# Performance work log

Measured on AMD Instinct MI355X. Metric: run time of the kernel, lower is better.

The kernel has to match this reference:

```python
import jax, jax.numpy as jnp
import numpy as np
from jax import lax

B, N, K = 8, 4096, 16          # clouds, points per cloud, knn neighbors
RATIO = 0.5
M = int(N * RATIO)             # sampled points per cloud (fps ratio)
C_IN, C_OUT = 64, 128
EPS = 1e-5                      # BatchNorm eps


def setup_inputs() -> dict:
    key = jax.random.key(0)
    ks = jax.random.split(key, 4)
    x = jax.random.normal(ks[0], (B * N, C_IN), jnp.float32)
    pos = jax.random.uniform(ks[1], (B * N, 3), jnp.float32)
    batch = jnp.repeat(jnp.arange(B, dtype=jnp.int32), N)
    W = jax.random.normal(ks[2], (C_IN, C_OUT), jnp.float32) / np.sqrt(C_IN).astype(np.float32)
    b = jnp.zeros((C_OUT,), jnp.float32)
    gamma = jnp.ones((C_OUT,), jnp.float32)
    beta = jnp.zeros((C_OUT,), jnp.float32)
    return {"x": x, "pos": pos, "batch": batch, "W": W, "b": b, "gamma": gamma, "beta": beta}


def _fps(pos_c):
    # Farthest point sampling on one cloud. pos_c: [N,3] -> [M] local indices.
    # Deterministic start at index 0 (reference for torch_cluster.fps).
    def step(carry, _):
        dmin, last = carry
        d = jnp.sum((pos_c - pos_c[last]) ** 2, axis=-1)   # [N]
        dmin = jnp.minimum(dmin, d)
        nxt = jnp.argmax(dmin).astype(jnp.int32)
        return (dmin, nxt), last
    init = (jnp.full((pos_c.shape[0],), jnp.inf, pos_c.dtype), jnp.int32(0))
    _, idx = lax.scan(step, init, None, length=M)
    return idx


def _knn(pos_c, qpos_c):
    # k nearest original points for each sampled point. [N,3],[M,3] -> [M,K].
    d = jnp.sum((qpos_c[:, None, :] - pos_c[None, :, :]) ** 2, axis=-1)  # [M,N]
    _, idx = lax.top_k(-d, K)
    return idx


def reference(x, pos, batch, W, b, gamma, beta):
    pos_b = pos.reshape(B, N, 3)
    fps_idx = jax.vmap(_fps)(pos_b)                                       # [B,M]
    new_pos_b = jnp.take_along_axis(pos_b, fps_idx[:, :, None], axis=1)   # [B,M,3]
    nbr = jax.vmap(_knn)(pos_b, new_pos_b)                                # [B,M,K]

    # mlp: Linear -> BatchNorm1d (training-mode batch stats) -> GELU
    h = x @ W + b                                                         # [B*N,C_OUT]
    mu = jnp.mean(h, axis=0)
    var = jnp.mean((h - mu) ** 2, axis=0)
    h = (h - mu) * lax.rsqrt(var + EPS) * gamma + beta
    h = jax.nn.gelu(h, approximate=False)
    h_b = h.reshape(B, N, C_OUT)

    # gather neighbor features; scatter-max over edge_index[0] == max over K
    # (each sampled point has exactly K incoming edges)
    feats = jax.vmap(lambda hb, nb: hb[nb])(h_b, nbr)                     # [B,M,K,C_OUT]
    new_x = jnp.max(feats, axis=2).reshape(B * M, C_OUT)
    new_pos = new_pos_b.reshape(B * M, 3)
    new_batch = jnp.repeat(jnp.arange(B, dtype=batch.dtype), M)
    return (new_x, new_pos, new_batch)
```

## Files before the change

### kernel.cpp

```cpp
#include <hip/hip_runtime.h>
#include <math.h>

#define NB 8
#define NN 4096
#define MM 2048
#define KNN_K 16
#define CIN 64
#define COUT 128
#define BN_EPS 1e-5f
#define NWORK 128
#define NTILES 512

typedef float v2f __attribute__((ext_vector_type(2)));

__device__ __forceinline__ v2f pk_add(v2f a, v2f b) {
  v2f r;
  asm("v_pk_add_f32 %0, %1, %2" : "=v"(r) : "v"(a), "v"(b));
  return r;
}
__device__ __forceinline__ v2f pk_mul(v2f a, v2f b) {
  v2f r;
  asm("v_pk_mul_f32 %0, %1, %2" : "=v"(r) : "v"(a), "v"(b));
  return r;
}

__device__ __forceinline__ double pack_key(float d, unsigned code) {
  return __longlong_as_double(
      (long long)(((unsigned long long)__float_as_uint(d) << 32) | code));
}
__device__ __forceinline__ unsigned unpack_code(double v) {
  return (unsigned)((unsigned long long)__double_as_longlong(v) &
                    0xFFFFFFFFull);
}

__device__ __forceinline__ float sqdist_np(float dx, float dy, float dz) {
  return __fadd_rn(__fadd_rn(__fmul_rn(dx, dx), __fmul_rn(dy, dy)),
                   __fmul_rn(dz, dz));
}

__device__ __forceinline__ void bar_lds_only() {
  asm volatile("s_waitcnt lgkmcnt(0)\n\ts_barrier" ::: "memory");
}

#define DPP_MAX_LEVEL(best, ctrl, rmask)                                     \
  {                                                                          \
    const int _lo = __builtin_amdgcn_update_dpp(                             \
        __double2loint(best), __double2loint(best), (ctrl), (rmask), 0xf,    \
        false);                                                              \
    const int _hi = __builtin_amdgcn_update_dpp(                             \
        __double2hiint(best), __double2hiint(best), (ctrl), (rmask), 0xf,    \
        false);                                                              \
    best = fmax(best, __hiloint2double(_hi, _lo));                           \
  }
#define DPP_MIN_LEVEL(best, ctrl, rmask)                                     \
  {                                                                          \
    const int _lo = __builtin_amdgcn_update_dpp(                             \
        __double2loint(best), __double2loint(best), (ctrl), (rmask), 0xf,    \
        false);                                                              \
    const int _hi = __builtin_amdgcn_update_dpp(                             \
        __double2hiint(best), __double2hiint(best), (ctrl), (rmask), 0xf,    \
        false);                                                              \
    best = fmin(best, __hiloint2double(_hi, _lo));                           \
  }

__device__ __forceinline__ float gelu_exact(float v) {
  return 0.5f * v * (1.0f + erff(v * 0.70710678118654752f));
}

__global__ __launch_bounds__(256) void k_fused(
    const float* __restrict__ pos, const float* __restrict__ x,
    const float* __restrict__ W, const float* __restrict__ bias,
    const float* __restrict__ gamma, const float* __restrict__ beta,
    float* __restrict__ h, float* __restrict__ gsum,
    float* __restrict__ gsumsq, int* __restrict__ pub,
    int* __restrict__ gemm_done, float* __restrict__ out_x,
    float* __restrict__ out_pos, float* __restrict__ out_batch) {
  __shared__ __align__(16) char smem_raw[50176];
  const int tid = threadIdx.x;
  const int lane = tid & 63, wv = tid >> 6;

  if (blockIdx.x < NB) {
    __builtin_amdgcn_s_setprio(3);
    float* xs = (float*)smem_raw;
    float* ys = xs + NN;
    float* zs = ys + NN;
    double* red = (double*)(smem_raw + 49152);
    const int b = blockIdx.x;
    const float* posc = pos + (size_t)b * NN * 3;
    for (int i = tid; i < NN; i += 256) {
      xs[i] = posc[i * 3 + 0];
      ys[i] = posc[i * 3 + 1];
      zs[i] = posc[i * 3 + 2];
    }
    __syncthreads();

    v2f pxv[8], pyv[8], pzv[8];
    double key[16];
    const unsigned code_base = (unsigned)(NN - 1 - tid * 16);
#pragma unroll
    for (int u = 0; u < 8; ++u) {
      const int p = tid * 16 + 2 * u;
      pxv[u] = (v2f){xs[p], xs[p + 1]};
      pyv[u] = (v2f){ys[p], ys[p + 1]};
      pzv[u] = (v2f){zs[p], zs[p + 1]};
    }
#pragma unroll
    for (int s = 0; s < 16; ++s)
      key[s] = __hiloint2double(0x7f800000, (int)(code_base - s));

    int last = 0;
    float lx = xs[0], ly = ys[0], lz = zs[0];
    if (tid == 0) {
      __hip_atomic_store(&pub[b * MM], 1, __ATOMIC_RELAXED,
                         __HIP_MEMORY_SCOPE_AGENT);
      out_pos[(size_t)(b * MM) * 3 + 0] = lx;
      out_pos[(size_t)(b * MM) * 3 + 1] = ly;
      out_pos[(size_t)(b * MM) * 3 + 2] = lz;
    }
    for (int m = 1; m < MM; ++m) {
      const v2f nlx = {-lx, -lx}, nly = {-ly, -ly}, nlz = {-lz, -lz};
      double b0 = 0.0, b1 = 0.0, b2 = 0.0, b3 = 0.0;
#pragma unroll
      for (int u = 0; u < 8; ++u) {
        const v2f dx = pk_add(pxv[u], nlx);
        const v2f dy = pk_add(pyv[u], nly);
        const v2f dz = pk_add(pzv[u], nlz);
        const v2f d2 =
            pk_add(pk_add(pk_mul(dx, dx), pk_mul(dy, dy)), pk_mul(dz, dz));
        const int s0 = 2 * u, s1 = 2 * u + 1;
        const float n0 =
            fminf(__int_as_float(__double2hiint(key[s0])), d2.x);
        const float n1 =
            fminf(__int_as_float(__double2hiint(key[s1])), d2.y);
        key[s0] = __hiloint2double(__float_as_int(n0), (int)(code_base - s0));
        key[s1] = __hiloint2double(__float_as_int(n1), (int)(code_base - s1));
        switch (u & 3) {
          case 0: b0 = fmax(b0, fmax(key[s0], key[s1])); break;
          case 1: b1 = fmax(b1, fmax(key[s0], key[s1])); break;
          case 2: b2 = fmax(b2, fmax(key[s0], key[s1])); break;
          default: b3 = fmax(b3, fmax(key[s0], key[s1])); break;
        }
      }
      double best = fmax(fmax(b0, b1), fmax(b2, b3));
      DPP_MAX_LEVEL(best, 0x121, 0xf);
      DPP_MAX_LEVEL(best, 0x122, 0xf);
      DPP_MAX_LEVEL(best, 0x124, 0xf);
      DPP_MAX_LEVEL(best, 0x128, 0xf);
      DPP_MAX_LEVEL(best, 0x142, 0xa);
      DPP_MAX_LEVEL(best, 0x143, 0xc);
      const int par = (m & 1) * 4;
      if (lane == 63) red[par + wv] = best;
      bar_lds_only();
      const double f = fmax(fmax(red[par + 0], red[par + 1]),
                            fmax(red[par + 2], red[par + 3]));
      last = (NN - 1) - (int)unpack_code(f);
      lx = xs[last];
      ly = ys[last];
      lz = zs[last];
      if (tid == 0) {
        const int o = b * MM + m;
        __hip_atomic_store(&pub[o], last + 1, __ATOMIC_RELAXED,
                           __HIP_MEMORY_SCOPE_AGENT);
        out_pos[(size_t)o * 3 + 0] = lx;
        out_pos[(size_t)o * 3 + 1] = ly;
        out_pos[(size_t)o * 3 + 2] = lz;
      }
    }
    __builtin_amdgcn_s_setprio(0);
    for (int m = tid; m < MM; m += 256) out_batch[b * MM + m] = (float)b;
  } else {
    const int wkr = blockIdx.x - NB;
    float* Wl = (float*)smem_raw;
    float* xl = Wl + CIN * COUT;
    float* bsum = (float*)(smem_raw + 49152);
    float* bsq = bsum + COUT;
    for (int i = tid; i < CIN * COUT; i += 256) Wl[i] = W[i];
#pragma unroll 1
    for (int rep = 0; rep < 4; ++rep) {
      const int t = wkr + rep * NWORK;
      const int r0 = t * 64;
      for (int i = tid; i < 64 * CIN; i += 256)
        xl[i] = x[(size_t)r0 * CIN + i];
      bsum[tid] = 0.f;
      __syncthreads();
      const int cg = tid & 31, rg = tid >> 5;
      const int c = cg * 4;
      float acc[8][4];
#pragma unroll
      for (int j = 0; j < 8; ++j)
#pragma unroll
        for (int tt = 0; tt < 4; ++tt) acc[j][tt] = 0.f;
      for (int k = 0; k < CIN; ++k) {
        const float4 wk = *(const float4*)&Wl[k * COUT + c];
#pragma unroll
        for (int j = 0; j < 8; ++j) {
          const float xv = xl[(rg * 8 + j) * CIN + k];
          acc[j][0] = fmaf(xv, wk.x, acc[j][0]);
          acc[j][1] = fmaf(xv, wk.y, acc[j][1]);
          acc[j][2] = fmaf(xv, wk.z, acc[j][2]);
          acc[j][3] = fmaf(xv, wk.w, acc[j][3]);
        }
      }
      const float4 bb = *(const float4*)&bias[c];
      float s0 = 0, s1 = 0, s2 = 0, s3 = 0, q0 = 0, q1 = 0, q2 = 0, q3 = 0;
#pragma unroll
      for (int j = 0; j < 8; ++j) {
        float4 hv;
        hv.x = acc[j][0] + bb.x;
        hv.y = acc[j][1] + bb.y;
        hv.z = acc[j][2] + bb.z;
        hv.w = acc[j][3] + bb.w;
        *(float4*)&h[(size_t)(r0 + rg * 8 + j) * COUT + c] = hv;
        s0 += hv.x; s1 += hv.y; s2 += hv.z; s3 += hv.w;
        q0 += hv.x * hv.x; q1 += hv.y * hv.y;
        q2 += hv.z * hv.z; q3 += hv.w * hv.w;
      }
      atomicAdd(&bsum[c + 0], s0); atomicAdd(&bsum[c + 1], s1);
      atomicAdd(&bsum[c + 2], s2); atomicAdd(&bsum[c + 3], s3);
      atomicAdd(&bsq[c + 0], q0);  atomicAdd(&bsq[c + 1], q1);
      atomicAdd(&bsq[c + 2], q2);  atomicAdd(&bsq[c + 3], q3);
      __syncthreads();
      if (tid < COUT) {
        atomicAdd(&gsum[tid], bsum[tid]);
        atomicAdd(&gsumsq[tid], bsq[tid]);
      }
      __syncthreads();
      if (tid == 0) {
        __threadfence();
        atomicAdd(gemm_done, 1);
      }
    }

    const int b = wkr & 7;
    float* px = (float*)smem_raw;
    float* py = px + NN;
    float* pz = py + NN;
    const float* posc = pos + (size_t)b * NN * 3;
    for (int i = tid; i < NN; i += 256) {
      px[i] = posc[i * 3 + 0];
      py[i] = posc[i * 3 + 1];
      pz[i] = posc[i * 3 + 2];
    }

    if (tid == 0) {
      while (__hip_atomic_load(gemm_done, __ATOMIC_RELAXED,
                               __HIP_MEMORY_SCOPE_AGENT) < NTILES)
        __builtin_amdgcn_s_sleep(64);
    }
    __syncthreads();
    __threadfence();

    float* scs = (float*)(smem_raw + 49152);
    float* shs = scs + COUT;
    if (tid < COUT) {
      const float n = (float)(NB * NN);
      const float su = __hip_atomic_load(&gsum[tid], __ATOMIC_RELAXED,
                                         __HIP_MEMORY_SCOPE_AGENT);
      const float sq = __hip_atomic_load(&gsumsq[tid], __ATOMIC_RELAXED,
                                         __HIP_MEMORY_SCOPE_AGENT);
      const float mu = su / n;
      const float var = sq / n - mu * mu;
      const float rs = rsqrtf(var + BN_EPS);
      const float s = rs * gamma[tid];
      scs[tid] = s;
      shs[tid] = beta[tid] - mu * s;
    }
    __syncthreads();

    const int widx = (wkr >> 3) * 4 + wv;
    const float sc0 = scs[lane], sh0 = shs[lane];
    const float sc1 = scs[lane + 64], sh1 = shs[lane + 64];
    const double DINF = __longlong_as_double(0x7FF0000000000000LL);
    const float PINF = __int_as_float(0x7f800000);
    const float* hb = h + (size_t)b * NN * COUT;
    const int* pubc = pub + b * MM;

    for (int m = widx; m < MM; m += 64) {
      int pv = __hip_atomic_load(&pubc[m], __ATOMIC_RELAXED,
                                 __HIP_MEMORY_SCOPE_AGENT);
      if (pv == 0) {
        __builtin_amdgcn_s_sleep(8);
        pv = __hip_atomic_load(&pubc[m], __ATOMIC_RELAXED,
                               __HIP_MEMORY_SCOPE_AGENT);
        while (pv == 0) {
          __builtin_amdgcn_s_sleep(96);
          pv = __hip_atomic_load(&pubc[m], __ATOMIC_RELAXED,
                                 __HIP_MEMORY_SCOPE_AGENT);
        }
      }
      const int qi = pv - 1;
      const float qx = px[qi], qy = py[qi], qz = pz[qi];
      double gmin[8];
#pragma unroll
      for (int g = 0; g < 8; ++g) gmin[g] = DINF;
      unsigned long long rm = 0ull;
#pragma unroll
      for (int s = 0; s < 64; ++s) {
        const int p = (s << 6) + lane;
        const float d = sqdist_np(px[p] - qx, py[p] - qy, pz[p] - qz);
        gmin[s >> 3] = fmin(gmin[s >> 3], pack_key(d, (unsigned)p));
      }
      double lmin = gmin[0];
#pragma unroll
      for (int g = 1; g < 8; ++g) lmin = fmin(lmin, gmin[g]);

      int nbr[KNN_K];
#pragma unroll
      for (int r = 0; r < KNN_K; ++r) {
        double v = lmin;
        DPP_MIN_LEVEL(v, 0x121, 0xf);
        DPP_MIN_LEVEL(v, 0x122, 0xf);
        DPP_MIN_LEVEL(v, 0x124, 0xf);
        DPP_MIN_LEVEL(v, 0x128, 0xf);
        DPP_MIN_LEVEL(v, 0x142, 0xa);
        DPP_MIN_LEVEL(v, 0x143, 0xc);
        const unsigned p =
            (unsigned)__builtin_amdgcn_readlane(__double2loint(v), 63);
        nbr[r] = (int)p;
        if (lane == (int)(p & 63)) {
          const int sr = (int)(p >> 6);
          rm |= (1ull << sr);
          const int g = sr >> 3;
          double nm = DINF;
#pragma unroll
          for (int j = 0; j < 8; ++j) {
            const int s2 = (g << 3) + j;
            const int pp = (s2 << 6) + lane;
            const float d =
                sqdist_np(px[pp] - qx, py[pp] - qy, pz[pp] - qz);
            double kk = pack_key(d, (unsigned)pp);
            if ((rm >> s2) & 1ull) kk = DINF;
            nm = fmin(nm, kk);
          }
#pragma unroll
          for (int gg = 0; gg < 8; ++gg)
            if (gg == g) gmin[gg] = nm;
          lmin = gmin[0];
#pragma unroll
          for (int gg = 1; gg < 8; ++gg) lmin = fmin(lmin, gmin[gg]);
        }
      }

      float mx0 = -PINF, mn0 = PINF, mx1 = -PINF, mn1 = PINF;
#pragma unroll
      for (int r = 0; r < KNN_K; ++r) {
        const float* row = hb + (size_t)nbr[r] * COUT;
        const float a = row[lane], cc = row[lane + 64];
        mx0 = fmaxf(mx0, a);
        mn0 = fminf(mn0, a);
        mx1 = fmaxf(mx1, cc);
        mn1 = fminf(mn1, cc);
      }
      const int q = b * MM + m;
      const float o0 = fmaxf(gelu_exact(fmaf(mx0, sc0, sh0)),
                             gelu_exact(fmaf(mn0, sc0, sh0)));
      const float o1 = fmaxf(gelu_exact(fmaf(mx1, sc1, sh1)),
                             gelu_exact(fmaf(mn1, sc1, sh1)));
      out_x[(size_t)q * COUT + lane] = o0;
      out_x[(size_t)q * COUT + lane + 64] = o1;
    }
  }
}

extern "C" void kernel_launch(void* const* d_in, const int* in_sizes, int n_in,
                              void* d_out, int out_size, void* d_ws,
                              size_t ws_size, hipStream_t stream) {
  const float* x = (const float*)d_in[0];
  const float* pos = (const float*)d_in[1];
  const float* W = (const float*)d_in[3];
  const float* bias = (const float*)d_in[4];
  const float* gamma = (const float*)d_in[5];
  const float* beta = (const float*)d_in[6];

  float* out_x = (float*)d_out;
  float* out_pos = out_x + (size_t)NB * MM * COUT;
  float* out_batch = out_pos + (size_t)NB * MM * 3;

  char* ws = (char*)d_ws;
  float* h = (float*)ws;
  float* gsum = (float*)(ws + (size_t)16777216);
  float* gsumsq = gsum + COUT;
  int* pub = (int*)(gsumsq + COUT);
  int* gemm_done = pub + NB * MM;

  (void)hipMemsetAsync(gsum, 0, 2 * COUT * sizeof(float) +
                                     NB * MM * sizeof(int) + sizeof(int),
                       stream);
  hipLaunchKernelGGL(k_fused, dim3(NB + NWORK), dim3(256), 0, stream, pos, x,
                     W, bias, gamma, beta, h, gsum, gsumsq, pub, gemm_done,
                     out_x, out_pos, out_batch);
}
```

Before: 1.207 ms.

## Add fifth wavefront to offload FPS result publishing and widen kNN workers

Blocks grow to 320 threads. In the FPS blocks, a dedicated fifth wave takes over publishing each sampled index and writing out_pos, so the four compute waves no longer stall on global stores inside the serial loop. In the worker blocks, the extra wave only helps during the kNN/gather phase, which now uses 5 waves per block with an 80-point stride. The GEMM still uses only 256 threads. The extra wave's barrier participation and higher register pressure could slow the latency-critical FPS loop.

Measured after the change: 1.160 ms (median of 2 runs). 3.9% less time.

```diff
diff --git a/kernel.cpp b/kernel.cpp
--- a/kernel.cpp
+++ b/kernel.cpp
@@ -10,6 +10,7 @@
 #define BN_EPS 1e-5f
 #define NWORK 128
 #define NTILES 512
+#define BT 320
 
 typedef float v2f __attribute__((ext_vector_type(2)));
 
@@ -67,7 +68,7 @@
   return 0.5f * v * (1.0f + erff(v * 0.70710678118654752f));
 }
 
-__global__ __launch_bounds__(256) void k_fused(
+__global__ __launch_bounds__(BT) void k_fused(
     const float* __restrict__ pos, const float* __restrict__ x,
     const float* __restrict__ W, const float* __restrict__ bias,
     const float* __restrict__ gamma, const float* __restrict__ beta,
@@ -87,138 +88,153 @@
     double* red = (double*)(smem_raw + 49152);
     const int b = blockIdx.x;
     const float* posc = pos + (size_t)b * NN * 3;
-    for (int i = tid; i < NN; i += 256) {
+    for (int i = tid; i < NN; i += BT) {
       xs[i] = posc[i * 3 + 0];
       ys[i] = posc[i * 3 + 1];
       zs[i] = posc[i * 3 + 2];
     }
     __syncthreads();
 
-    v2f pxv[8], pyv[8], pzv[8];
-    double key[16];
-    const unsigned code_base = (unsigned)(NN - 1 - tid * 16);
-#pragma unroll
-    for (int u = 0; u < 8; ++u) {
-      const int p = tid * 16 + 2 * u;
-      pxv[u] = (v2f){xs[p], xs[p + 1]};
-      pyv[u] = (v2f){ys[p], ys[p + 1]};
-      pzv[u] = (v2f){zs[p], zs[p + 1]};
-    }
-#pragma unroll
-    for (int s = 0; s < 16; ++s)
-      key[s] = __hiloint2double(0x7f800000, (int)(code_base - s));
-
-    int last = 0;
-    float lx = xs[0], ly = ys[0], lz = zs[0];
-    if (tid == 0) {
-      __hip_atomic_store(&pub[b * MM], 1, __ATOMIC_RELAXED,
-                         __HIP_MEMORY_SCOPE_AGENT);
-      out_pos[(size_t)(b * MM) * 3 + 0] = lx;
-      out_pos[(size_t)(b * MM) * 3 + 1] = ly;
-      out_pos[(size_t)(b * MM) * 3 + 2] = lz;
-    }
-    for (int m = 1; m < MM; ++m) {
-      const v2f nlx = {-lx, -lx}, nly = {-ly, -ly}, nlz = {-lz, -lz};
-      double b0 = 0.0, b1 = 0.0, b2 = 0.0, b3 = 0.0;
+    if (tid < 256) {
+      v2f pxv[8], pyv[8], pzv[8];
+      double key[16];
+      const unsigned code_base = (unsigned)(NN - 1 - tid * 16);
 #pragma unroll
       for (int u = 0; u < 8; ++u) {
-        const v2f dx = pk_add(pxv[u], nlx);
-        const v2f dy = pk_add(pyv[u], nly);
-        const v2f dz = pk_add(pzv[u], nlz);
-        const v2f d2 =
-            pk_add(pk_add(pk_mul(dx, dx), pk_mul(dy, dy)), pk_mul(dz, dz));
-        const int s0 = 2 * u, s1 = 2 * u + 1;
-        const float n0 =
-            fminf(__int_as_float(__double2hiint(key[s0])), d2.x);
-        const float n1 =
-            fminf(__int_as_float(__double2hiint(key[s1])), d2.y);
-        key[s0] = __hiloint2double(__float_as_int(n0), (int)(code_base - s0));
-        key[s1] = __hiloint2double(__float_as_int(n1), (int)(code_base - s1));
-        switch (u & 3) {
-          case 0: b0 = fmax(b0, fmax(key[s0], key[s1])); break;
-          case 1: b1 = fmax(b1, fmax(key[s0], key[s1])); break;
-          case 2: b2 = fmax(b2, fmax(key[s0], key[s1])); break;
-          default: b3 = fmax(b3, fmax(key[s0], key[s1])); break;
-        }
-      }
-      double best = fmax(fmax(b0, b1), fmax(b2, b3));
-      DPP_MAX_LEVEL(best, 0x121, 0xf);
-      DPP_MAX_LEVEL(best, 0x122, 0xf);
-      DPP_MAX_LEVEL(best, 0x124, 0xf);
-      DPP_MAX_LEVEL(best, 0x128, 0xf);
-      DPP_MAX_LEVEL(best, 0x142, 0xa);
-      DPP_MAX_LEVEL(best, 0x143, 0xc);
-      const int par = (m & 1) * 4;
-      if (lane == 63) red[par + wv] = best;
-      bar_lds_only();
-      const double f = fmax(fmax(red[par + 0], red[par + 1]),
-                            fmax(red[par + 2], red[par + 3]));
-      last = (NN - 1) - (int)unpack_code(f);
-      lx = xs[last];
-      ly = ys[last];
-      lz = zs[last];
-      if (tid == 0) {
-        const int o = b * MM + m;
-        __hip_atomic_store(&pub[o], last + 1, __ATOMIC_RELAXED,
+        const int p = tid * 16 + 2 * u;
+        pxv[u] = (v2f){xs[p], xs[p + 1]};
+        pyv[u] = (v2f){ys[p], ys[p + 1]};
+        pzv[u] = (v2f){zs[p], zs[p + 1]};
+      }
+#pragma unroll
+      for (int s = 0; s < 16; ++s)
+        key[s] = __hiloint2double(0x7f800000, (int)(code_base - s));
+
+      int last = 0;
+      float lx = xs[0], ly = ys[0], lz = zs[0];
+      for (int m = 1; m < MM; ++m) {
+        const v2f nlx = {-lx, -lx}, nly = {-ly, -ly}, nlz = {-lz, -lz};
+        double b0 = 0.0, b1 = 0.0, b2 = 0.0, b3 = 0.0;
+#pragma unroll
+        for (int u = 0; u < 8; ++u) {
+          const v2f dx = pk_add(pxv[u], nlx);
+          const v2f dy = pk_add(pyv[u], nly);
+          const v2f dz = pk_add(pzv[u], nlz);
+          const v2f d2 =
+              pk_add(pk_add(pk_mul(dx, dx), pk_mul(dy, dy)), pk_mul(dz, dz));
+          const int s0 = 2 * u, s1 = 2 * u + 1;
+          const float n0 =
+              fminf(__int_as_float(__double2hiint(key[s0])), d2.x);
+          const float n1 =
+              fminf(__int_as_float(__double2hiint(key[s1])), d2.y);
+          key[s0] =
+              __hiloint2double(__float_as_int(n0), (int)(code_base - s0));
+          key[s1] =
+              __hiloint2double(__float_as_int(n1), (int)(code_base - s1));
+          switch (u & 3) {
+            case 0: b0 = fmax(b0, fmax(key[s0], key[s1])); break;
+            case 1: b1 = fmax(b1, fmax(key[s0], key[s1])); break;
+            case 2: b2 = fmax(b2, fmax(key[s0], key[s1])); break;
+            default: b3 = fmax(b3, fmax(key[s0], key[s1])); break;
+          }
+        }
+        double best = fmax(fmax(b0, b1), fmax(b2, b3));
+        DPP_MAX_LEVEL(best, 0x121, 0xf);
+        DPP_MAX_LEVEL(best, 0x122, 0xf);
+        DPP_MAX_LEVEL(best, 0x124, 0xf);
+        DPP_MAX_LEVEL(best, 0x128, 0xf);
+        DPP_MAX_LEVEL(best, 0x142, 0xa);
+        DPP_MAX_LEVEL(best, 0x143, 0xc);
+        const int par = (m & 1) * 4;
+        if (lane == 63) red[par + wv] = best;
+        bar_lds_only();
+        const double f = fmax(fmax(red[par + 0], red[par + 1]),
+                              fmax(red[par + 2], red[par + 3]));
+        last = (NN - 1) - (int)unpack_code(f);
+        lx = xs[last];
+        ly = ys[last];
+        lz = zs[last];
+      }
+      (void)last;
+    } else {
+      if (tid == 256) {
+        __hip_atomic_store(&pub[b * MM], 1, __ATOMIC_RELAXED,
                            __HIP_MEMORY_SCOPE_AGENT);
-        out_pos[(size_t)o * 3 + 0] = lx;
-        out_pos[(size_t)o * 3 + 1] = ly;
-        out_pos[(size_t)o * 3 + 2] = lz;
+        out_pos[(size_t)(b * MM) * 3 + 0] = xs[0];
+        out_pos[(size_t)(b * MM) * 3 + 1] = ys[0];
+        out_pos[(size_t)(b * MM) * 3 + 2] = zs[0];
+      }
+      for (int m = 1; m < MM; ++m) {
+        bar_lds_only();
+        if (tid == 256) {
+          const int par = (m & 1) * 4;
+          const double f = fmax(fmax(red[par + 0], red[par + 1]),
+                                fmax(red[par + 2], red[par + 3]));
+          const int last = (NN - 1) - (int)unpack_code(f);
+          const int o = b * MM + m;
+          __hip_atomic_store(&pub[o], last + 1, __ATOMIC_RELAXED,
+                             __HIP_MEMORY_SCOPE_AGENT);
+          out_pos[(size_t)o * 3 + 0] = xs[last];
+          out_pos[(size_t)o * 3 + 1] = ys[last];
+          out_pos[(size_t)o * 3 + 2] = zs[last];
+        }
       }
     }
     __builtin_amdgcn_s_setprio(0);
-    for (int m = tid; m < MM; m += 256) out_batch[b * MM + m] = (float)b;
+    for (int m = tid; m < MM; m += BT) out_batch[b * MM + m] = (float)b;
   } else {
     const int wkr = blockIdx.x - NB;
     float* Wl = (float*)smem_raw;
     float* xl = Wl + CIN * COUT;
     float* bsum = (float*)(smem_raw + 49152);
     float* bsq = bsum + COUT;
-    for (int i = tid; i < CIN * COUT; i += 256) Wl[i] = W[i];
+    for (int i = tid; i < CIN * COUT; i += BT) Wl[i] = W[i];
 #pragma unroll 1
     for (int rep = 0; rep < 4; ++rep) {
       const int t = wkr + rep * NWORK;
       const int r0 = t * 64;
-      for (int i = tid; i < 64 * CIN; i += 256)
+      for (int i = tid; i < 64 * CIN; i += BT)
         xl[i] = x[(size_t)r0 * CIN + i];
-      bsum[tid] = 0.f;
+      if (tid < 256) bsum[tid] = 0.f;
       __syncthreads();
-      const int cg = tid & 31, rg = tid >> 5;
-      const int c = cg * 4;
-      float acc[8][4];
-#pragma unroll
-      for (int j = 0; j < 8; ++j)
-#pragma unroll
-        for (int tt = 0; tt < 4; ++tt) acc[j][tt] = 0.f;
-      for (int k = 0; k < CIN; ++k) {
-        const float4 wk = *(const float4*)&Wl[k * COUT + c];
+      if (tid < 256) {
+        const int cg = tid & 31, rg = tid >> 5;
+        const int c = cg * 4;
+        float acc[8][4];
+#pragma unroll
+        for (int j = 0; j < 8; ++j)
+#pragma unroll
+          for (int tt = 0; tt < 4; ++tt) acc[j][tt] = 0.f;
+        for (int k = 0; k < CIN; ++k) {
+          const float4 wk = *(const float4*)&Wl[k * COUT + c];
+#pragma unroll
+          for (int j = 0; j < 8; ++j) {
+            const float xv = xl[(rg * 8 + j) * CIN + k];
+            acc[j][0] = fmaf(xv, wk.x, acc[j][0]);
+            acc[j][1] = fmaf(xv, wk.y, acc[j][1]);
+            acc[j][2] = fmaf(xv, wk.z, acc[j][2]);
+            acc[j][3] = fmaf(xv, wk.w, acc[j][3]);
+          }
+        }
+        const float4 bb = *(const float4*)&bias[c];
+        float s0 = 0, s1 = 0, s2 = 0, s3 = 0, q0 = 0, q1 = 0, q2 = 0, q3 = 0;
 #pragma unroll
         for (int j = 0; j < 8; ++j) {
-          const float xv = xl[(rg * 8 + j) * CIN + k];
-          acc[j][0] = fmaf(xv, wk.x, acc[j][0]);
-          acc[j][1] = fmaf(xv, wk.y, acc[j][1]);
-          acc[j][2] = fmaf(xv, wk.z, acc[j][2]);
-          acc[j][3] = fmaf(xv, wk.w, acc[j][3]);
-        }
-      }
-      const float4 bb = *(const float4*)&bias[c];
-      float s0 = 0, s1 = 0, s2 = 0, s3 = 0, q0 = 0, q1 = 0, q2 = 0, q3 = 0;
-#pragma unroll
-      for (int j = 0; j < 8; ++j) {
-        float4 hv;
-        hv.x = acc[j][0] + bb.x;
-        hv.y = acc[j][1] + bb.y;
-        hv.z = acc[j][2] + bb.z;
-        hv.w = acc[j][3] + bb.w;
-        *(float4*)&h[(size_t)(r0 + rg * 8 + j) * COUT + c] = hv;
-        s0 += hv.x; s1 += hv.y; s2 += hv.z; s3 += hv.w;
-        q0 += hv.x * hv.x; q1 += hv.y * hv.y;
-        q2 += hv.z * hv.z; q3 += hv.w * hv.w;
-      }
-      atomicAdd(&bsum[c + 0], s0); atomicAdd(&bsum[c + 1], s1);
-      atomicAdd(&bsum[c + 2], s2); atomicAdd(&bsum[c + 3], s3);
-      atomicAdd(&bsq[c + 0], q0);  atomicAdd(&bsq[c + 1], q1);
-      atomicAdd(&bsq[c + 2], q2);  atomicAdd(&bsq[c + 3], q3);
+          float4 hv;
+          hv.x = acc[j][0] + bb.x;
+          hv.y = acc[j][1] + bb.y;
+          hv.z = acc[j][2] + bb.z;
+          hv.w = acc[j][3] + bb.w;
+          *(float4*)&h[(size_t)(r0 + rg * 8 + j) * COUT + c] = hv;
+          s0 += hv.x; s1 += hv.y; s2 += hv.z; s3 += hv.w;
+          q0 += hv.x * hv.x; q1 += hv.y * hv.y;
+          q2 += hv.z * hv.z; q3 += hv.w * hv.w;
+        }
+        atomicAdd(&bsum[c + 0], s0); atomicAdd(&bsum[c + 1], s1);
+        atomicAdd(&bsum[c + 2], s2); atomicAdd(&bsum[c + 3], s3);
+        atomicAdd(&bsq[c + 0], q0);  atomicAdd(&bsq[c + 1], q1);
+        atomicAdd(&bsq[c + 2], q2);  atomicAdd(&bsq[c + 3], q3);
+      }
       __syncthreads();
       if (tid < COUT) {
         atomicAdd(&gsum[tid], bsum[tid]);
@@ -236,7 +252,7 @@
     float* py = px + NN;
     float* pz = py + NN;
     const float* posc = pos + (size_t)b * NN * 3;
-    for (int i = tid; i < NN; i += 256) {
+    for (int i = tid; i < NN; i += BT) {
       px[i] = posc[i * 3 + 0];
       py[i] = posc[i * 3 + 1];
       pz[i] = posc[i * 3 + 2];
@@ -267,7 +283,7 @@
     }
     __syncthreads();
 
-    const int widx = (wkr >> 3) * 4 + wv;
+    const int widx = (wkr >> 3) * 5 + wv;
     const float sc0 = scs[lane], sh0 = shs[lane];
     const float sc1 = scs[lane + 64], sh1 = shs[lane + 64];
     const double DINF = __longlong_as_double(0x7FF0000000000000LL);
@@ -275,7 +291,7 @@
     const float* hb = h + (size_t)b * NN * COUT;
     const int* pubc = pub + b * MM;
 
-    for (int m = widx; m < MM; m += 64) {
+    for (int m = widx; m < MM; m += 80) {
       int pv = __hip_atomic_load(&pubc[m], __ATOMIC_RELAXED,
                                  __HIP_MEMORY_SCOPE_AGENT);
       if (pv == 0) {
@@ -386,7 +402,7 @@
   (void)hipMemsetAsync(gsum, 0, 2 * COUT * sizeof(float) +
                                      NB * MM * sizeof(int) + sizeof(int),
                        stream);
-  hipLaunchKernelGGL(k_fused, dim3(NB + NWORK), dim3(256), 0, stream, pos, x,
+  hipLaunchKernelGGL(k_fused, dim3(NB + NWORK), dim3(BT), 0, stream, pos, x,
                      W, bias, gamma, beta, h, gsum, gsumsq, pub, gemm_done,
                      out_x, out_pos, out_batch);
 }
```
